# Optimization experiments

Measured on AMD Instinct MI355X. Metric: run time of the kernel, lower is better.

The kernel has to match this reference:

```python
import jax, jax.numpy as jnp
import numpy as np

B, N, D_OBJ, D_Q, D_FUSED, D_BOX, D_ATT = 64, 36, 2048, 2048, 2048, 4, 512


def setup_inputs() -> dict:
    key = jax.random.key(0)
    ks = jax.random.split(key, 12)
    s = lambda d: 1.0 / np.sqrt(d)
    return {
        "question_embedding": jax.random.normal(ks[0], (B * N, D_Q), jnp.float32),
        "object_features_list": jax.random.normal(ks[1], (B, N, D_OBJ), jnp.float32),
        "bounding_boxes": jax.random.uniform(ks[2], (B, N, D_BOX), jnp.float32),
        "Wq": jax.random.normal(ks[3], (D_Q, D_FUSED), jnp.float32) * s(D_Q),
        "Wo": jax.random.normal(ks[4], (D_OBJ, D_FUSED), jnp.float32) * s(D_OBJ),
        "Wfa": jax.random.normal(ks[5], (D_FUSED, D_FUSED), jnp.float32) * s(D_FUSED),
        "Wfb": jax.random.normal(ks[6], (D_FUSED, D_FUSED), jnp.float32) * s(D_FUSED),
        "Wba": jax.random.normal(ks[7], (D_BOX, D_FUSED), jnp.float32) * s(D_BOX),
        "Wbb": jax.random.normal(ks[8], (D_BOX, D_FUSED), jnp.float32) * s(D_BOX),
        "W0": jax.random.normal(ks[9], (D_FUSED, D_ATT), jnp.float32) * s(D_FUSED),
        "b0": jnp.zeros((D_ATT,), jnp.float32),
        "W1": jax.random.normal(ks[10], (D_ATT, 1), jnp.float32) * s(D_ATT),
        "b1": jnp.zeros((1,), jnp.float32),
        "batch_size": B,
        "num_obj": N,
    }


def reference(question_embedding, object_features_list, bounding_boxes,
              Wq, Wo, Wfa, Wfb, Wba, Wbb, W0, b0, W1, b1,
              batch_size, num_obj):
    # fuse_object_features_with_questions: MLB fusion of question and objects
    obj_flat = object_features_list.reshape(batch_size * num_obj, -1)  # [BN, D]
    fused = (question_embedding @ Wq) * (obj_flat @ Wo)                # [BN, Df]
    fused = fused.reshape(batch_size, num_obj, -1)                     # [B, N, Df]

    # pairwise: project once, broadcast-multiply instead of materializing
    # expanded [B*N*N, D] operands (same math as expand+view+fusion).
    ra = fused @ Wfa                 # [B, N, Df]
    rb = fused @ Wfb                 # [B, N, Df]
    ba = bounding_boxes @ Wba        # [B, N, Df]
    bb = bounding_boxes @ Wbb        # [B, N, Df]
    # relations[b, i, j, :] = fusion_fused(f_i, f_j) + fusion_box(box_i, box_j)
    relations = ra[:, :, None, :] * rb[:, None, :, :] + ba[:, :, None, :] * bb[:, None, :, :]  # [B,N,N,Df]

    # compute_relation_attention: linear-tanh-linear, softmax over dim=2
    h = jnp.tanh(relations @ W0 + b0)          # [B, N, N, D_att]
    scores = h @ W1 + b1                       # [B, N, N, 1]
    att = jax.nn.softmax(scores, axis=2)[..., 0]  # [B, N, N]
    e_hat = jnp.sum(relations * att[..., None], axis=2)  # [B, N, Df]

    pairwise_res = fused + e_hat
    return object_features_list + pairwise_res
```

## Files before the change

kernel.cpp:

```cpp
#include <hip/hip_runtime.h>
#include <hip/hip_bf16.h>
#include <math.h>

constexpr int kB    = 64;
constexpr int kN    = 36;
constexpr int kBN   = kB * kN;
constexpr int kD    = 2048;
constexpr int kDatt = 512;
constexpr int kPairs = kN * kN;
constexpr int kRows  = kB * kPairs;

using bf16x8 = __attribute__((ext_vector_type(8))) short;
using f32x4  = __attribute__((ext_vector_type(4))) float;

typedef unsigned int u32;
typedef __attribute__((address_space(3))) u32 lds_u32;
typedef const __attribute__((address_space(1))) u32 glb_u32;

__device__ inline unsigned short f2bf(float f) {
    union { float f; unsigned u; } v; v.f = f;
    unsigned r = v.u + 0x7FFFu + ((v.u >> 16) & 1u);
    return (unsigned short)(r >> 16);
}

__global__ __launch_bounds__(256)
void kcvt(const float* __restrict__ x, unsigned short* __restrict__ y, int n4)
{
    int i = blockIdx.x * 256 + threadIdx.x;
    if (i < n4) {
        float4 v = ((const float4*)x)[i];
        ushort4 o = {f2bf(v.x), f2bf(v.y), f2bf(v.z), f2bf(v.w)};
        ((ushort4*)y)[i] = o;
    }
}

__global__ __launch_bounds__(256)
void ktrp(const float* __restrict__ W, unsigned short* __restrict__ WT, int nt)
{
    __shared__ float T[64][65];
    const int k0 = blockIdx.x * 64;
    const int n0 = blockIdx.y * 64;
    const int c = threadIdx.x & 63, r0 = threadIdx.x >> 6;
    #pragma unroll
    for (int rr = 0; rr < 64; rr += 4)
        T[r0 + rr][c] = W[(size_t)(k0 + r0 + rr) * nt + n0 + c];
    __syncthreads();
    #pragma unroll
    for (int rr = 0; rr < 64; rr += 4)
        WT[(size_t)(n0 + r0 + rr) * kD + k0 + c] = f2bf(T[c][r0 + rr]);
}

__global__ __launch_bounds__(64)
void krepack_w0(const unsigned short* __restrict__ W0T, unsigned short* __restrict__ W0s)
{
    const int kb    = blockIdx.x;
    const int chunk = blockIdx.y;
    const int g     = threadIdx.x;
    const int row = chunk * 16 + (g & 7) + ((g >> 5) << 3);
    const int cg8 = ((g >> 3) & 3) * 8;
    const uint4 v = *(const uint4*)&W0T[(size_t)row * kD + kb * 32 + cg8];
    *(uint4*)&W0s[(size_t)kb * 16384 + chunk * 512 + g * 8] = v;
}

__global__ __launch_bounds__(256)
void k3_box_proj(const float* __restrict__ box, const float* __restrict__ Wba,
                 const float* __restrict__ Wbb,
                 float* __restrict__ ba, float* __restrict__ bb)
{
    const int r = blockIdx.y;
    const int c = blockIdx.x * 256 + threadIdx.x;
    const float x0 = box[r * 4 + 0], x1 = box[r * 4 + 1];
    const float x2 = box[r * 4 + 2], x3 = box[r * 4 + 3];
    float va = x0 * Wba[c] + x1 * Wba[kD + c] + x2 * Wba[2 * kD + c] + x3 * Wba[3 * kD + c];
    float vb = x0 * Wbb[c] + x1 * Wbb[kD + c] + x2 * Wbb[2 * kD + c] + x3 * Wbb[3 * kD + c];
    ba[(size_t)r * kD + c] = va;
    bb[(size_t)r * kD + c] = vb;
}

__device__ inline void stage128(const unsigned short* __restrict__ g,
                                int grow0, int k0,
                                unsigned short* lds, int w, int lane)
{
    const int sr = lane >> 2, sc = (lane & 3) * 8;
    #pragma unroll
    for (int t = 0; t < 2; ++t) {
        int r = w * 32 + t * 16;
        const unsigned short* gp = g + (size_t)(grow0 + r + sr) * kD + k0 + sc;
        __builtin_amdgcn_global_load_lds((glb_u32*)gp, (lds_u32*)(lds + r * 32), 16, 0, 0);
    }
}
__device__ inline void stage64(const unsigned short* __restrict__ g,
                               int grow0, int k0,
                               unsigned short* lds, int w, int lane)
{
    const int sr = lane >> 2, sc = (lane & 3) * 8;
    int r = w * 16;
    const unsigned short* gp = g + (size_t)(grow0 + r + sr) * kD + k0 + sc;
    __builtin_amdgcn_global_load_lds((glb_u32*)gp, (lds_u32*)(lds + r * 32), 16, 0, 0);
}

__global__ __launch_bounds__(256, 2)
void k1_dual_mfma(const unsigned short* __restrict__ Qb,
                  const unsigned short* __restrict__ WqT,
                  const unsigned short* __restrict__ Ob,
                  const unsigned short* __restrict__ WoT,
                  unsigned short* __restrict__ fusedb)
{
    __shared__ __align__(16) unsigned short As1[128][32];
    __shared__ __align__(16) unsigned short As2[128][32];
    __shared__ __align__(16) unsigned short Bs1[64][32];
    __shared__ __align__(16) unsigned short Bs2[64][32];

    const int tid = threadIdx.x;
    const int lane = tid & 63;
    const int w = tid >> 6;
    const int wm = w >> 1, wn = w & 1;
    const int row0 = blockIdx.y * 128;
    const int col0 = blockIdx.x * 64;

    f32x4 acc1[4][2], acc2[4][2];
    #pragma unroll
    for (int mt = 0; mt < 4; ++mt)
        #pragma unroll
        for (int nt = 0; nt < 2; ++nt) { acc1[mt][nt] = (f32x4)(0.f); acc2[mt][nt] = (f32x4)(0.f); }

    const int fr = lane & 15, ko = (lane >> 4) * 8;

    for (int k0 = 0; k0 < kD; k0 += 32) {
        stage128(Qb,  row0, k0, &As1[0][0], w, lane);
        stage128(Ob,  row0, k0, &As2[0][0], w, lane);
        stage64 (WqT, col0, k0, &Bs1[0][0], w, lane);
        stage64 (WoT, col0, k0, &Bs2[0][0], w, lane);
        __syncthreads();

        bf16x8 a1[4], a2[4];
        #pragma unroll
        for (int mt = 0; mt < 4; ++mt) {
            a1[mt] = *(bf16x8*)&As1[wm * 64 + mt * 16 + fr][ko];
            a2[mt] = *(bf16x8*)&As2[wm * 64 + mt * 16 + fr][ko];
        }
        #pragma unroll
        for (int nt = 0; nt < 2; ++nt) {
            bf16x8 b1 = *(bf16x8*)&Bs1[wn * 32 + nt * 16 + fr][ko];
            bf16x8 b2 = *(bf16x8*)&Bs2[wn * 32 + nt * 16 + fr][ko];
            #pragma unroll
            for (int mt = 0; mt < 4; ++mt) {
                acc1[mt][nt] = __builtin_amdgcn_mfma_f32_16x16x32_bf16(a1[mt], b1, acc1[mt][nt], 0, 0, 0);
                acc2[mt][nt] = __builtin_amdgcn_mfma_f32_16x16x32_bf16(a2[mt], b2, acc2[mt][nt], 0, 0, 0);
            }
        }
        __syncthreads();
    }

    const int fq = lane >> 4;
    #pragma unroll
    for (int mt = 0; mt < 4; ++mt)
        #pragma unroll
        for (int nt = 0; nt < 2; ++nt) {
            int row = row0 + wm * 64 + mt * 16 + fq * 4;
            int col = col0 + wn * 32 + nt * 16 + fr;
            #pragma unroll
            for (int reg = 0; reg < 4; ++reg) {
                float v = acc1[mt][nt][reg] * acc2[mt][nt][reg];
                fusedb[(size_t)(row + reg) * kD + col] = f2bf(v);
            }
        }
}

__global__ __launch_bounds__(256, 2)
void k2_dual_mfma(const unsigned short* __restrict__ Fb,
                  const unsigned short* __restrict__ WfaT,
                  const unsigned short* __restrict__ WfbT,
                  float* __restrict__ ra, float* __restrict__ rb)
{
    __shared__ __align__(16) unsigned short As [128][32];
    __shared__ __align__(16) unsigned short Bs1[64][32];
    __shared__ __align__(16) unsigned short Bs2[64][32];

    const int tid = threadIdx.x;
    const int lane = tid & 63;
    const int w = tid >> 6;
    const int wm = w >> 1, wn = w & 1;
    const int row0 = blockIdx.y * 128;
    const int col0 = blockIdx.x * 64;

    f32x4 acc1[4][2], acc2[4][2];
    #pragma unroll
    for (int mt = 0; mt < 4; ++mt)
        #pragma unroll
        for (int nt = 0; nt < 2; ++nt) { acc1[mt][nt] = (f32x4)(0.f); acc2[mt][nt] = (f32x4)(0.f); }

    const int fr = lane & 15, ko = (lane >> 4) * 8;

    for (int k0 = 0; k0 < kD; k0 += 32) {
        stage128(Fb,   row0, k0, &As [0][0], w, lane);
        stage64 (WfaT, col0, k0, &Bs1[0][0], w, lane);
        stage64 (WfbT, col0, k0, &Bs2[0][0], w, lane);
        __syncthreads();

        bf16x8 a[4];
        #pragma unroll
        for (int mt = 0; mt < 4; ++mt)
            a[mt] = *(bf16x8*)&As[wm * 64 + mt * 16 + fr][ko];
        #pragma unroll
        for (int nt = 0; nt < 2; ++nt) {
            bf16x8 b1 = *(bf16x8*)&Bs1[wn * 32 + nt * 16 + fr][ko];
            bf16x8 b2 = *(bf16x8*)&Bs2[wn * 32 + nt * 16 + fr][ko];
            #pragma unroll
            for (int mt = 0; mt < 4; ++mt) {
                acc1[mt][nt] = __builtin_amdgcn_mfma_f32_16x16x32_bf16(a[mt], b1, acc1[mt][nt], 0, 0, 0);
                acc2[mt][nt] = __builtin_amdgcn_mfma_f32_16x16x32_bf16(a[mt], b2, acc2[mt][nt], 0, 0, 0);
            }
        }
        __syncthreads();
    }

    const int fq = lane >> 4;
    #pragma unroll
    for (int mt = 0; mt < 4; ++mt)
        #pragma unroll
        for (int nt = 0; nt < 2; ++nt) {
            int row = row0 + wm * 64 + mt * 16 + fq * 4;
            int col = col0 + wn * 32 + nt * 16 + fr;
            #pragma unroll
            for (int reg = 0; reg < 4; ++reg) {
                size_t o = (size_t)(row + reg) * kD + col;
                ra[o] = acc1[mt][nt][reg];
                rb[o] = acc2[mt][nt][reg];
            }
        }
}

__global__ __launch_bounds__(512, 2)
void k4_scores_mfma(const float* __restrict__ ra, const float* __restrict__ rb,
                    const float* __restrict__ ba, const float* __restrict__ bb,
                    const unsigned short* __restrict__ W0s,
                    const float* __restrict__ b0, const float* __restrict__ W1,
                    float* __restrict__ scores)
{
    __shared__ __align__(16) unsigned short Bs[2][512 * 32];
    __shared__ __align__(16) unsigned short RelS[2][128][40];
    __shared__ float scoreS[128];

    const int tid  = threadIdx.x;
    const int lane = tid & 63;
    const int w    = tid >> 6;
    const int wm   = w >> 2;
    const int wn   = w & 3;
    const int t0   = blockIdx.x * 128;

    int rowA[2], cgA[2];
    const float *raP[2], *rbP[2], *baP[2], *bbP[2];
    #pragma unroll
    for (int t = 0; t < 2; ++t) {
        int s = tid + t * 512;
        rowA[t] = s >> 3; cgA[t] = s & 7;
        int gp = t0 + rowA[t];
        int b  = gp / kPairs;
        int r  = gp - b * kPairs;
        int i  = r / kN, j = r - i * kN;
        raP[t] = ra + (size_t)(b * kN + i) * kD;
        baP[t] = ba + (size_t)(b * kN + i) * kD;
        rbP[t] = rb + (size_t)(b * kN + j) * kD;
        bbP[t] = bb + (size_t)(b * kN + j) * kD;
    }

    const int fr = lane & 15, fq = lane >> 4;
    const int bco = ((fr & 7) << 3) + ((fr >> 3) << 8) + (fq << 6);

    f32x4 acc[4][8];
    #pragma unroll
    for (int mt = 0; mt < 4; ++mt)
        #pragma unroll
        for (int nt = 0; nt < 8; ++nt)
            acc[mt][nt] = (f32x4)(0.f);

    if (tid < 128) scoreS[tid] = 0.f;

    float4 pa[2], pr[2], pp[2], pq[2];

    #define ISSUE_B(k0_, buf_)                                                   \
        _Pragma("unroll")                                                        \
        for (int t = 0; t < 4; ++t) {                                            \
            int chunk = w * 4 + t;                                               \
            const unsigned short* gp = W0s + (size_t)((k0_) >> 5) * 16384        \
                                       + chunk * 512 + lane * 8;                 \
            __builtin_amdgcn_global_load_lds((glb_u32*)gp,                       \
                (lds_u32*)&Bs[buf_][chunk * 512], 16, 0, 0);                     \
        }

    #define LOAD_A(k0_)                                                          \
        _Pragma("unroll")                                                        \
        for (int t = 0; t < 2; ++t) {                                            \
            pa[t] = *(const float4*)(raP[t] + (k0_) + cgA[t] * 4);               \
            pr[t] = *(const float4*)(rbP[t] + (k0_) + cgA[t] * 4);               \
            pp[t] = *(const float4*)(baP[t] + (k0_) + cgA[t] * 4);               \
            pq[t] = *(const float4*)(bbP[t] + (k0_) + cgA[t] * 4);               \
        }

    #define WRITE_REL(buf_)                                                      \
        _Pragma("unroll")                                                        \
        for (int t = 0; t < 2; ++t) {                                            \
            ushort4 o;                                                           \
            o.x = f2bf(pa[t].x * pr[t].x + pp[t].x * pq[t].x);                   \
            o.y = f2bf(pa[t].y * pr[t].y + pp[t].y * pq[t].y);                   \
            o.z = f2bf(pa[t].z * pr[t].z + pp[t].z * pq[t].z);                   \
            o.w = f2bf(pa[t].w * pr[t].w + pp[t].w * pq[t].w);                   \
            *(ushort4*)&RelS[buf_][rowA[t]][cgA[t] * 4] = o;                     \
        }

    LOAD_A(0)
    ISSUE_B(0, 0)
    WRITE_REL(0)

    for (int k0 = 0; k0 < kD; k0 += 32) {
        const int cur = (k0 >> 5) & 1, nxt = cur ^ 1;
        const bool more = (k0 + 32 < kD);
        __syncthreads();
        if (more) {
            LOAD_A(k0 + 32)
            ISSUE_B(k0 + 32, nxt)
        }
        bf16x8 af[4];
        #pragma unroll
        for (int mt = 0; mt < 4; ++mt)
            af[mt] = *(bf16x8*)&RelS[cur][wm * 64 + mt * 16 + fr][fq * 8];
        #pragma unroll
        for (int nt = 0; nt < 8; ++nt) {
            bf16x8 bfv = *(bf16x8*)&Bs[cur][wn * 4096 + nt * 512 + bco];
            #pragma unroll
            for (int mt = 0; mt < 4; ++mt)
                acc[mt][nt] = __builtin_amdgcn_mfma_f32_16x16x32_bf16(af[mt], bfv, acc[mt][nt], 0, 0, 0);
        }
        if (more) { WRITE_REL(nxt) }
    }

    float b0v[8], w1v[8];
    #pragma unroll
    for (int nt = 0; nt < 8; ++nt) {
        int col = wn * 128 + nt * 16 + fr;
        b0v[nt] = b0[col];
        w1v[nt] = W1[col];
    }
    #pragma unroll
    for (int mt = 0; mt < 4; ++mt) {
        #pragma unroll
        for (int reg = 0; reg < 4; ++reg) {
            float p = 0.f;
            #pragma unroll
            for (int nt = 0; nt < 8; ++nt)
                p += w1v[nt] * tanhf(acc[mt][nt][reg] + b0v[nt]);
            p += __shfl_xor(p, 1, 64);
            p += __shfl_xor(p, 2, 64);
            p += __shfl_xor(p, 4, 64);
            p += __shfl_xor(p, 8, 64);
            if (fr == 0)
                atomicAdd(&scoreS[wm * 64 + mt * 16 + fq * 4 + reg], p);
        }
    }
    __syncthreads();
    if (tid < 128)
        scores[(size_t)t0 + tid] = scoreS[tid];
}

__global__ __launch_bounds__(64)
void k5_softmax(const float* __restrict__ scores, float* __restrict__ att)
{
    const int bi = blockIdx.x;
    const int tid = threadIdx.x;
    float s = (tid < kN) ? scores[(size_t)bi * kN + tid] : -1e30f;
    float m = s;
    #pragma unroll
    for (int off = 32; off >= 1; off >>= 1)
        m = fmaxf(m, __shfl_xor(m, off, 64));
    float e = (tid < kN) ? expf(s - m) : 0.f;
    float sum = e;
    #pragma unroll
    for (int off = 32; off >= 1; off >>= 1)
        sum += __shfl_xor(sum, off, 64);
    if (tid < kN) att[(size_t)bi * kN + tid] = e / sum;
}

__global__ __launch_bounds__(256)
void k6_output(const float* __restrict__ obj, const unsigned short* __restrict__ fusedb,
               const float* __restrict__ ra, const float* __restrict__ ba,
               const float* __restrict__ rb, const float* __restrict__ bb,
               const float* __restrict__ att, float* __restrict__ out)
{
    __shared__ float attS[kN];
    const int bi = blockIdx.x;
    const int b = bi / kN;
    const int tid = threadIdx.x;
    if (tid < kN) attS[tid] = att[(size_t)bi * kN + tid];
    __syncthreads();
    for (int d = tid; d < kD; d += 256) {
        float s1 = 0.f, s2 = 0.f;
        #pragma unroll 4
        for (int j = 0; j < kN; ++j) {
            float a = attS[j];
            size_t rrow = (size_t)(b * kN + j) * kD + d;
            s1 = fmaf(a, rb[rrow], s1);
            s2 = fmaf(a, bb[rrow], s2);
        }
        size_t o = (size_t)bi * kD + d;
        float fv = __uint_as_float((u32)fusedb[o] << 16);
        out[o] = obj[o] + fv + ra[o] * s1 + ba[o] * s2;
    }
}

extern "C" void kernel_launch(void* const* d_in, const int* in_sizes, int n_in,
                              void* d_out, int out_size, void* d_ws, size_t ws_size,
                              hipStream_t stream)
{
    const float* q   = (const float*)d_in[0];
    const float* obj = (const float*)d_in[1];
    const float* box = (const float*)d_in[2];
    const float* Wq  = (const float*)d_in[3];
    const float* Wo  = (const float*)d_in[4];
    const float* Wfa = (const float*)d_in[5];
    const float* Wfb = (const float*)d_in[6];
    const float* Wba = (const float*)d_in[7];
    const float* Wbb = (const float*)d_in[8];
    const float* W0  = (const float*)d_in[9];
    const float* b0v = (const float*)d_in[10];
    const float* W1  = (const float*)d_in[11];
    float* out = (float*)d_out;

    const size_t nBD = (size_t)kBN * kD;
    float* ws = (float*)d_ws;
    size_t off = 0;
    float* ra     = ws + off; off += nBD;
    float* rb     = ws + off; off += nBD;
    float* ba     = ws + off; off += nBD;
    float* bb     = ws + off; off += nBD;
    float* scores = ws + off; off += (size_t)kBN * kN;
    float* att    = ws + off; off += (size_t)kBN * kN;

    unsigned short* us = (unsigned short*)(ws + off);
    size_t uoff = 0;
    unsigned short* W0T     = us + uoff; uoff += (size_t)kDatt * kD;
    unsigned short* W0s     = us + uoff; uoff += (size_t)kDatt * kD;
    unsigned short* q_bf    = us + uoff; uoff += nBD;
    unsigned short* obj_bf  = us + uoff; uoff += nBD;
    unsigned short* fusedbf = us + uoff; uoff += nBD;
    unsigned short* WqT     = us + uoff; uoff += (size_t)kD * kD;
    unsigned short* WoT     = us + uoff; uoff += (size_t)kD * kD;
    unsigned short* WfaT = q_bf;
    unsigned short* WfbT = obj_bf;

    const int n4 = (int)(nBD / 4);
    kcvt<<<dim3((n4 + 255) / 256), 256, 0, stream>>>(q,   q_bf,   n4);
    kcvt<<<dim3((n4 + 255) / 256), 256, 0, stream>>>(obj, obj_bf, n4);
    ktrp<<<dim3(32, 32), 256, 0, stream>>>(Wq, WqT, kD);
    ktrp<<<dim3(32, 32), 256, 0, stream>>>(Wo, WoT, kD);
    ktrp<<<dim3(32, 8),  256, 0, stream>>>(W0, W0T, kDatt);
    krepack_w0<<<dim3(kD / 32, kDatt / 16), 64, 0, stream>>>(W0T, W0s);
    k3_box_proj<<<dim3(kD / 256, kBN), 256, 0, stream>>>(box, Wba, Wbb, ba, bb);

    k1_dual_mfma<<<dim3(kD / 64, kBN / 128), 256, 0, stream>>>(q_bf, WqT, obj_bf, WoT, fusedbf);

    ktrp<<<dim3(32, 32), 256, 0, stream>>>(Wfa, WfaT, kD);
    ktrp<<<dim3(32, 32), 256, 0, stream>>>(Wfb, WfbT, kD);

    k2_dual_mfma<<<dim3(kD / 64, kBN / 128), 256, 0, stream>>>(fusedbf, WfaT, WfbT, ra, rb);

    k4_scores_mfma<<<dim3(kRows / 128), 512, 0, stream>>>(ra, rb, ba, bb, W0s, b0v, W1, scores);
    k5_softmax<<<kBN, 64, 0, stream>>>(scores, att);
    k6_output<<<kBN, 256, 0, stream>>>(obj, fusedbf, ra, ba, rb, bb, att, out);
}
```

Measured before the change: 745.5 us.

## Stage per-batch ra/rb/ba/bb rows in LDS and build relations from shared tiles

```diff
diff --git a/kernel.cpp b/kernel.cpp
--- a/kernel.cpp
+++ b/kernel.cpp
@@ -8,7 +8,6 @@
 constexpr int kD    = 2048;
 constexpr int kDatt = 512;
 constexpr int kPairs = kN * kN;
-constexpr int kRows  = kB * kPairs;
 
 using bf16x8 = __attribute__((ext_vector_type(8))) short;
 using f32x4  = __attribute__((ext_vector_type(4))) float;
@@ -240,6 +239,7 @@
 {
     __shared__ __align__(16) unsigned short Bs[2][512 * 32];
     __shared__ __align__(16) unsigned short RelS[2][128][40];
+    __shared__ __align__(16) float4 Stg4[2][714];
     __shared__ float scoreS[128];
 
     const int tid  = threadIdx.x;
@@ -247,22 +247,48 @@
     const int w    = tid >> 6;
     const int wm   = w >> 2;
     const int wn   = w & 3;
-    const int t0   = blockIdx.x * 128;
-
-    int rowA[2], cgA[2];
-    const float *raP[2], *rbP[2], *baP[2], *bbP[2];
+
+    const int work = (blockIdx.x & 7) * 88 + (blockIdx.x >> 3);
+    const int b    = work / 11;
+    const int tile = work - b * 11;
+    const int p0   = tile * 128;
+    const int i0   = p0 / kN;
+
+    const float* raB = ra + (size_t)b * kN * kD;
+    const float* rbB = rb + (size_t)b * kN * kD;
+    const float* baB = ba + (size_t)b * kN * kD;
+    const float* bbB = bb + (size_t)b * kN * kD;
+
+    const bool has2 = (tid < 160);
+    const float* sptr[2];
+    int sdst[2];
+    #pragma unroll
+    for (int t = 0; t < 2; ++t) {
+        int s = tid + t * 512; if (s > 671) s = 671;
+        int row = s >> 4, t4 = s & 15;
+        int arr = t4 >> 3, q = t4 & 7;
+        int grow; const float* base;
+        if (row < 6) {
+            int il = (row < 5) ? row : 4;
+            grow = i0 + il; if (grow > kN - 1) grow = kN - 1;
+            base = arr ? baB : raB;
+        } else {
+            grow = row - 6;
+            base = arr ? bbB : rbB;
+        }
+        sptr[t] = base + (size_t)grow * kD + q * 4;
+        sdst[t] = row * 17 + t4;
+    }
+
+    int rowA[2], cgA[2], ilA[2], jA[2];
     #pragma unroll
     for (int t = 0; t < 2; ++t) {
         int s = tid + t * 512;
         rowA[t] = s >> 3; cgA[t] = s & 7;
-        int gp = t0 + rowA[t];
-        int b  = gp / kPairs;
-        int r  = gp - b * kPairs;
-        int i  = r / kN, j = r - i * kN;
-        raP[t] = ra + (size_t)(b * kN + i) * kD;
-        baP[t] = ba + (size_t)(b * kN + i) * kD;
-        rbP[t] = rb + (size_t)(b * kN + j) * kD;
-        bbP[t] = bb + (size_t)(b * kN + j) * kD;
+        int p = p0 + rowA[t]; if (p >= kPairs) p = kPairs - 1;
+        int i = p / kN;
+        jA[t]  = p - i * kN;
+        ilA[t] = i - i0;
     }
 
     const int fr = lane & 15, fq = lane >> 4;
@@ -277,7 +303,7 @@
 
     if (tid < 128) scoreS[tid] = 0.f;
 
-    float4 pa[2], pr[2], pp[2], pq[2];
+    float4 sreg0, sreg1;
 
     #define ISSUE_B(k0_, buf_)                                                   \
         _Pragma("unroll")                                                        \
@@ -289,38 +315,44 @@
                 (lds_u32*)&Bs[buf_][chunk * 512], 16, 0, 0);                     \
         }
 
-    #define LOAD_A(k0_)                                                          \
+    #define STAGE_LOAD(k0_) {                                                    \
+            sreg0 = *(const float4*)(sptr[0] + (k0_));                           \
+            if (has2) sreg1 = *(const float4*)(sptr[1] + (k0_));                 \
+        }
+
+    #define STAGE_WRITE(buf_) {                                                  \
+            Stg4[buf_][sdst[0]] = sreg0;                                         \
+            if (has2) Stg4[buf_][sdst[1]] = sreg1;                               \
+        }
+
+    #define REL_GEN(buf_)                                                        \
         _Pragma("unroll")                                                        \
         for (int t = 0; t < 2; ++t) {                                            \
-            pa[t] = *(const float4*)(raP[t] + (k0_) + cgA[t] * 4);               \
-            pr[t] = *(const float4*)(rbP[t] + (k0_) + cgA[t] * 4);               \
-            pp[t] = *(const float4*)(baP[t] + (k0_) + cgA[t] * 4);               \
-            pq[t] = *(const float4*)(bbP[t] + (k0_) + cgA[t] * 4);               \
-        }
-
-    #define WRITE_REL(buf_)                                                      \
-        _Pragma("unroll")                                                        \
-        for (int t = 0; t < 2; ++t) {                                            \
+            float4 va = Stg4[buf_][ilA[t] * 17 + cgA[t]];                        \
+            float4 vb = Stg4[buf_][ilA[t] * 17 + 8 + cgA[t]];                    \
+            float4 vr = Stg4[buf_][(6 + jA[t]) * 17 + cgA[t]];                   \
+            float4 vq = Stg4[buf_][(6 + jA[t]) * 17 + 8 + cgA[t]];               \
             ushort4 o;                                                           \
-            o.x = f2bf(pa[t].x * pr[t].x + pp[t].x * pq[t].x);                   \
-            o.y = f2bf(pa[t].y * pr[t].y + pp[t].y * pq[t].y);                   \
-            o.z = f2bf(pa[t].z * pr[t].z + pp[t].z * pq[t].z);                   \
-            o.w = f2bf(pa[t].w * pr[t].w + pp[t].w * pq[t].w);                   \
+            o.x = f2bf(va.x * vr.x + vb.x * vq.x);                               \
+            o.y = f2bf(va.y * vr.y + vb.y * vq.y);                               \
+            o.z = f2bf(va.z * vr.z + vb.z * vq.z);                               \
+            o.w = f2bf(va.w * vr.w + vb.w * vq.w);                               \
             *(ushort4*)&RelS[buf_][rowA[t]][cgA[t] * 4] = o;                     \
         }
 
-    LOAD_A(0)
+    STAGE_LOAD(0)
+    STAGE_WRITE(0)
+    STAGE_LOAD(32)
+    __syncthreads();
+    REL_GEN(0)
+    STAGE_WRITE(1)
     ISSUE_B(0, 0)
-    WRITE_REL(0)
-
-    for (int k0 = 0; k0 < kD; k0 += 32) {
-        const int cur = (k0 >> 5) & 1, nxt = cur ^ 1;
-        const bool more = (k0 + 32 < kD);
+
+    for (int k = 0; k < 64; ++k) {
+        const int cur = k & 1, nxt = cur ^ 1;
         __syncthreads();
-        if (more) {
-            LOAD_A(k0 + 32)
-            ISSUE_B(k0 + 32, nxt)
-        }
+        if (k < 62) STAGE_LOAD((k + 2) * 32)
+        if (k < 63) ISSUE_B((k + 1) * 32, nxt)
         bf16x8 af[4];
         #pragma unroll
         for (int mt = 0; mt < 4; ++mt)
@@ -332,7 +364,8 @@
             for (int mt = 0; mt < 4; ++mt)
                 acc[mt][nt] = __builtin_amdgcn_mfma_f32_16x16x32_bf16(af[mt], bfv, acc[mt][nt], 0, 0, 0);
         }
-        if (more) { WRITE_REL(nxt) }
+        if (k < 62) STAGE_WRITE(cur)
+        if (k < 63) REL_GEN(nxt)
     }
 
     float b0v[8], w1v[8];
@@ -359,8 +392,8 @@
         }
     }
     __syncthreads();
-    if (tid < 128)
-        scores[(size_t)t0 + tid] = scoreS[tid];
+    if (tid < 128 && p0 + tid < kPairs)
+        scores[(size_t)b * kPairs + p0 + tid] = scoreS[tid];
 }
 
 __global__ __launch_bounds__(64)
@@ -464,7 +497,7 @@
 
     k2_dual_mfma<<<dim3(kD / 64, kBN / 128), 256, 0, stream>>>(fusedbf, WfaT, WfbT, ra, rb);
 
-    k4_scores_mfma<<<dim3(kRows / 128), 512, 0, stream>>>(ra, rb, ba, bb, W0s, b0v, W1, scores);
+    k4_scores_mfma<<<dim3(kB * 11), 512, 0, stream>>>(ra, rb, ba, bb, W0s, b0v, W1, scores);
     k5_softmax<<<kBN, 64, 0, stream>>>(scores, att);
     k6_output<<<kBN, 256, 0, stream>>>(obj, fusedbf, ra, ba, rb, bb, att, out);
 }
```

New measurement: 712.8 us. -4.4%, faster.
